# Kernel tuning notes

Hardware: AMD Instinct MI355X
Metric: run time of the kernel (lower is better)

## Reference

```python
import jax, jax.numpy as jnp
import numpy as np

NUM_HEADS = 12


def setup_inputs() -> dict:
    key = jax.random.key(0)
    ks = jax.random.split(key, 5)
    B, N, C = 4, 2048, 768
    s = 0.02
    return {
        "x": jax.random.normal(ks[0], (B, N, C), jnp.float32),
        "qkv_w": jax.random.normal(ks[1], (3 * C, C), jnp.float32) * s,
        "qkv_b": jax.random.normal(ks[2], (3 * C,), jnp.float32) * s,
        "proj_w": jax.random.normal(ks[3], (C, C), jnp.float32) * s,
        "proj_b": jax.random.normal(ks[4], (C,), jnp.float32) * s,
    }


def reference(x, qkv_w, qkv_b, proj_w, proj_b):
    B, N, C = x.shape
    H = NUM_HEADS
    D = C // H
    scale = D ** -0.5
    # qkv projection: [B,N,3C] -> [3,B,H,N,D]
    qkv = (x @ qkv_w.T + qkv_b).reshape(B, N, 3, H, D).transpose(2, 0, 3, 1, 4)
    q, k, v = qkv[0], qkv[1], qkv[2]
    attn = jnp.einsum("bhnd,bhmd->bhnm", q, k) * scale  # [B,H,N,N]
    attn_probs = jax.nn.softmax(attn, axis=-1)
    # dropout p=0 (eval) -> identity
    out = jnp.einsum("bhnm,bhmd->bhnd", attn_probs, v)  # [B,H,N,D]
    out = out.transpose(0, 2, 1, 3).reshape(B, N, C)
    return out @ proj_w.T + proj_b
```

## Files before the change

### kernel.cpp

```cpp
#include <hip/hip_runtime.h>

typedef __attribute__((ext_vector_type(8))) short bf16x8;
typedef __attribute__((ext_vector_type(4))) float f32x4;
typedef __attribute__((ext_vector_type(4))) unsigned int u32x4;
typedef __attribute__((ext_vector_type(2))) unsigned int u32x2;

#define QSCALE 0.1803368801111243f

__device__ inline unsigned short f2bf(float f) {
  union { float f; unsigned u; } v; v.f = f;
  unsigned r = v.u + 0x7fffu + ((v.u >> 16) & 1u);
  return (unsigned short)(r >> 16);
}

__device__ inline unsigned packbf2(float a, float b) {
  union { float f; unsigned u; } va, vb; va.f = a; vb.f = b;
  unsigned ta = va.u + 0x7fffu + ((va.u >> 16) & 1u);
  unsigned tb = vb.u + 0x7fffu + ((vb.u >> 16) & 1u);
  return __builtin_amdgcn_perm(tb, ta, 0x07060302);
}

__device__ inline void async16(const void* g, void* l) {
  __builtin_amdgcn_global_load_lds(
      (const __attribute__((address_space(1))) unsigned int*)g,
      (__attribute__((address_space(3))) unsigned int*)l, 16, 0, 0);
}

__device__ inline void cast8(const float* __restrict__ s, unsigned short* __restrict__ d) {
  float4 v0 = *(const float4*)s, v1 = *(const float4*)(s + 4);
  u32x4 o;
  o.x = packbf2(v0.x, v0.y); o.y = packbf2(v0.z, v0.w);
  o.z = packbf2(v1.x, v1.y); o.w = packbf2(v1.z, v1.w);
  *(u32x4*)d = o;
}

__global__ __launch_bounds__(256) void cast_x(const float* __restrict__ x,
                                              unsigned short* __restrict__ xs) {
  size_t idx = (size_t)blockIdx.x * 256 + threadIdx.x;
  cast8(x + idx * 8, xs + idx * 8);
}

__global__ __launch_bounds__(256) void cast_w(const float* __restrict__ wq,
                                              const float* __restrict__ wp,
                                              unsigned short* __restrict__ wqs,
                                              unsigned short* __restrict__ wps) {
  int idx = blockIdx.x * 256 + threadIdx.x;
  if (idx < 221184) cast8(wq + (size_t)idx * 8, wqs + (size_t)idx * 8);
  else {
    size_t j = (size_t)(idx - 221184) * 8;
    cast8(wp + j, wps + j);
  }
}

template<int MODE>
__global__ __launch_bounds__(256, 3) void gemm_lds(
    const unsigned short* __restrict__ A, const unsigned short* __restrict__ B,
    const float* __restrict__ bias,
    unsigned short* __restrict__ oq, unsigned short* __restrict__ ok,
    unsigned short* __restrict__ ov, float* __restrict__ of)
{
  constexpr int NI = (MODE == 0) ? 4 : 2;
  constexpr int TN = NI * 32;
  __shared__ unsigned short As[128 * 64];
  __shared__ unsigned short Bs[TN * 64];

  const int t = threadIdx.x, w = t >> 6, lane = t & 63;
  const int quad = lane >> 4, l16 = lane & 15;
  const int bm = blockIdx.x, bn = blockIdx.y;
  const int wr = w >> 1, wc = w & 1;

  const int r_off = lane >> 3;
  const int kb_lin = (lane & 7) << 4;

  const unsigned short* Ag = A + (size_t)(bm * 128) * 768;
  const unsigned short* Bg = B + (size_t)(bn * TN) * 768;

  const unsigned short* ApA[4]; unsigned short* LpA[4];
#pragma unroll
  for (int i = 0; i < 4; i++) {
    int r = w * 32 + i * 8 + r_off;
    int ks = (kb_lin ^ ((r & 7) << 4)) >> 1;
    ApA[i] = Ag + (size_t)r * 768 + ks;
    LpA[i] = As + (w * 32 + i * 8) * 64 + lane * 8;
  }
  const unsigned short* ApB[NI]; unsigned short* LpB[NI];
#pragma unroll
  for (int i = 0; i < NI; i++) {
    int r = w * (TN / 4) + i * 8 + r_off;
    int ks = (kb_lin ^ ((r & 7) << 4)) >> 1;
    ApB[i] = Bg + (size_t)r * 768 + ks;
    LpB[i] = Bs + (w * (TN / 4) + i * 8) * 64 + lane * 8;
  }

  f32x4 acc[4][NI] = {};
  const int swz = (l16 & 7) << 3;

  for (int kt = 0; kt < 12; kt++) {
    __syncthreads();
    const int k0 = kt * 64;
#pragma unroll
    for (int i = 0; i < 4; i++)  async16(ApA[i] + k0, LpA[i]);
#pragma unroll
    for (int i = 0; i < NI; i++) async16(ApB[i] + k0, LpB[i]);
    __syncthreads();

#pragma unroll
    for (int kc = 0; kc < 2; kc++) {
      const int ko = (kc * 32 + quad * 8) ^ swz;
      bf16x8 a[4], b[NI];
#pragma unroll
      for (int mi = 0; mi < 4; mi++)
        a[mi] = *(const bf16x8*)&As[(wr * 64 + mi * 16 + l16) * 64 + ko];
#pragma unroll
      for (int ni = 0; ni < NI; ni++)
        b[ni] = *(const bf16x8*)&Bs[(wc * (TN / 2) + ni * 16 + l16) * 64 + ko];
#pragma unroll
      for (int mi = 0; mi < 4; mi++)
#pragma unroll
        for (int ni = 0; ni < NI; ni++)
          acc[mi][ni] = __builtin_amdgcn_mfma_f32_16x16x32_bf16(a[mi], b[ni],
                                                                acc[mi][ni], 0, 0, 0);
    }
  }

  const int m_base = bm * 128 + wr * 64;
  if (MODE == 0) {
    const int three = (bn * TN) / 768;
    int hh[NI], dd[NI]; float bb[NI];
#pragma unroll
    for (int ni = 0; ni < NI; ni++) {
      int n_g = bn * TN + wc * (TN / 2) + ni * 16 + l16;
      bb[ni] = bias[n_g];
      int rem = n_g - three * 768;
      hh[ni] = rem >> 6; dd[ni] = rem & 63;
    }
    if (three == 2) {
#pragma unroll
      for (int ni = 0; ni < NI; ni++)
#pragma unroll
        for (int mi = 0; mi < 4; mi++) {
          int m0 = m_base + mi * 16 + (quad << 2);
          int b_ = m0 >> 11, ntok = m0 & 2047;
          u32x2 pv;
          pv.x = packbf2(acc[mi][ni][0] + bb[ni], acc[mi][ni][1] + bb[ni]);
          pv.y = packbf2(acc[mi][ni][2] + bb[ni], acc[mi][ni][3] + bb[ni]);
          *(u32x2*)(ov + (((size_t)b_ * 12 + hh[ni]) * 64 + dd[ni]) * 2048 + ntok) = pv;
        }
    } else {
      unsigned short* o = (three == 0) ? oq : ok;
      const float sc = (three == 0) ? QSCALE : 1.f;
#pragma unroll
      for (int mi = 0; mi < 4; mi++)
#pragma unroll
        for (int r = 0; r < 4; r++) {
          int m_g = m_base + mi * 16 + (quad << 2) + r;
          int b_ = m_g >> 11, ntok = m_g & 2047;
          size_t rowb = ((size_t)b_ * 12) * 2048;
#pragma unroll
          for (int ni = 0; ni < NI; ni++) {
            float v = (acc[mi][ni][r] + bb[ni]) * sc;
            o[((rowb + (size_t)hh[ni] * 2048 + ntok) << 6) + dd[ni]] = f2bf(v);
          }
        }
    }
  } else {
#pragma unroll
    for (int ni = 0; ni < NI; ni++) {
      int n_g = bn * TN + wc * (TN / 2) + ni * 16 + l16;
      float bs = bias[n_g];
#pragma unroll
      for (int mi = 0; mi < 4; mi++)
#pragma unroll
        for (int r = 0; r < 4; r++) {
          int m_g = m_base + mi * 16 + (quad << 2) + r;
          of[(size_t)m_g * 768 + n_g] = acc[mi][ni][r] + bs;
        }
    }
  }
}

__global__ __launch_bounds__(256, 3) void flash_attn(
    const unsigned short* __restrict__ Qb, const unsigned short* __restrict__ Kb,
    const unsigned short* __restrict__ Vtb, unsigned short* __restrict__ ao)
{
  __shared__ unsigned short Ks[2][4096];
  __shared__ unsigned short Vs[2][4096];
  const int t = threadIdx.x, w = t >> 6, lane = t & 63;
  const int quad = lane >> 4, l16 = lane & 15;
  const int bh = blockIdx.x, qt = blockIdx.y;
  const unsigned short* Qg = Qb + (size_t)bh * 2048 * 64;
  const unsigned short* Kg = Kb + (size_t)bh * 2048 * 64;
  const unsigned short* Vg = Vtb + (size_t)bh * 2048 * 64;

  bf16x8 bq[2][2];
#pragma unroll
  for (int u = 0; u < 2; u++) {
    int qrow = qt * 128 + w * 32 + u * 16 + l16;
#pragma unroll
    for (int h = 0; h < 2; h++)
      bq[u][h] = *(const bf16x8*)(Qg + (size_t)qrow * 64 + h * 32 + quad * 8);
  }

  const int s0 = t, s1 = 256 + t;
  auto gperm = [](int s) { return (s & 0x23) | ((s & 0x0c) << 1) | ((s & 0x10) >> 2); };
  const size_t koff0 = (size_t)gperm(s0 & 63) * 64 + (s0 >> 6) * 8;
  const size_t koff1 = (size_t)gperm(s1 & 63) * 64 + (s1 >> 6) * 8;
  const size_t voff0 = (size_t)(s0 & 63) * 2048 + (s0 >> 6) * 8;
  const size_t voff1 = (size_t)(s1 & 63) * 2048 + (s1 >> 6) * 8;

  float l_run[2] = {0.f, 0.f};
  f32x4 o_acc[2][4];
#pragma unroll
  for (int u = 0; u < 2; u++)
#pragma unroll
    for (int dt = 0; dt < 4; dt++) o_acc[u][dt] = (f32x4){0.f, 0.f, 0.f, 0.f};

  async16(Kg + koff0, &Ks[0][s0 * 8]);
  async16(Kg + koff1, &Ks[0][s1 * 8]);
  async16(Vg + voff0, &Vs[0][s0 * 8]);
  async16(Vg + voff1, &Vs[0][s1 * 8]);

  for (int kt = 0; kt < 32; kt++) {
    const int p = kt & 1;
    __syncthreads();
    if (kt < 31) {
      const unsigned short* Kn = Kg + (size_t)(kt + 1) * 4096;
      const unsigned short* Vn = Vg + (size_t)(kt + 1) * 64;
      async16(Kn + koff0, &Ks[p ^ 1][s0 * 8]);
      async16(Kn + koff1, &Ks[p ^ 1][s1 * 8]);
      async16(Vn + voff0, &Vs[p ^ 1][s0 * 8]);
      async16(Vn + voff1, &Vs[p ^ 1][s1 * 8]);
    }
    const unsigned short* Kp = &Ks[p][0];
    const unsigned short* Vp = &Vs[p][0];

    f32x4 sv[2][4];
#pragma unroll
    for (int nt = 0; nt < 4; nt++) {
      bf16x8 k0 = *(const bf16x8*)&Kp[((quad) * 64 + nt * 16 + l16) * 8];
      bf16x8 k1 = *(const bf16x8*)&Kp[((4 + quad) * 64 + nt * 16 + l16) * 8];
#pragma unroll
      for (int u = 0; u < 2; u++) {
        f32x4 s_ = {0.f, 0.f, 0.f, 0.f};
        s_ = __builtin_amdgcn_mfma_f32_16x16x32_bf16(k0, bq[u][0], s_, 0, 0, 0);
        s_ = __builtin_amdgcn_mfma_f32_16x16x32_bf16(k1, bq[u][1], s_, 0, 0, 0);
        sv[u][nt] = s_;
      }
    }

    union { unsigned u32[8]; bf16x8 v[2]; } pk[2];
#pragma unroll
    for (int u = 0; u < 2; u++) {
#pragma unroll
      for (int nt = 0; nt < 4; nt++) {
        float p0 = __builtin_amdgcn_exp2f(sv[u][nt][0]);
        float p1 = __builtin_amdgcn_exp2f(sv[u][nt][1]);
        float p2 = __builtin_amdgcn_exp2f(sv[u][nt][2]);
        float p3 = __builtin_amdgcn_exp2f(sv[u][nt][3]);
        l_run[u] += (p0 + p1) + (p2 + p3);
        pk[u].u32[nt * 2]     = packbf2(p0, p1);
        pk[u].u32[nt * 2 + 1] = packbf2(p2, p3);
      }
    }

#pragma unroll
    for (int cc = 0; cc < 2; cc++) {
#pragma unroll
      for (int dt = 0; dt < 4; dt++) {
        bf16x8 a = *(const bf16x8*)&Vp[((cc * 4 + quad) * 64 + dt * 16 + l16) * 8];
#pragma unroll
        for (int u = 0; u < 2; u++)
          o_acc[u][dt] = __builtin_amdgcn_mfma_f32_16x16x32_bf16(a, pk[u].v[cc], o_acc[u][dt], 0, 0, 0);
      }
    }
  }

  float linv[2];
#pragma unroll
  for (int u = 0; u < 2; u++) {
    float l = l_run[u];
    l += __shfl_xor(l, 16, 64);
    l += __shfl_xor(l, 32, 64);
    linv[u] = 1.f / l;
  }

  const int b_ = bh / 12, h = bh - b_ * 12;
#pragma unroll
  for (int u = 0; u < 2; u++) {
    int row = b_ * 2048 + qt * 128 + w * 32 + u * 16 + l16;
    unsigned short* base = ao + (size_t)row * 768 + h * 64 + (quad << 2);
#pragma unroll
    for (int dt = 0; dt < 4; dt++) {
      u32x2 pv;
      pv.x = packbf2(o_acc[u][dt][0] * linv[u], o_acc[u][dt][1] * linv[u]);
      pv.y = packbf2(o_acc[u][dt][2] * linv[u], o_acc[u][dt][3] * linv[u]);
      *(u32x2*)(base + dt * 16) = pv;
    }
  }
}

extern "C" void kernel_launch(void* const* d_in, const int* in_sizes, int n_in,
                              void* d_out, int out_size, void* d_ws, size_t ws_size,
                              hipStream_t stream) {
  const float* x      = (const float*)d_in[0];
  const float* qkv_w  = (const float*)d_in[1];
  const float* qkv_b  = (const float*)d_in[2];
  const float* proj_w = (const float*)d_in[3];
  const float* proj_b = (const float*)d_in[4];
  float* out = (float*)d_out;

  unsigned short* ws  = (unsigned short*)d_ws;
  unsigned short* wqs = ws;
  unsigned short* wps = wqs + 1769472;
  unsigned short* xs  = wps + 589824;
  unsigned short* qb  = xs + 6291456;
  unsigned short* kb  = qb + 6291456;
  unsigned short* vtb = kb + 6291456;
  unsigned short* ao  = vtb + 6291456;

  cast_w<<<1152, 256, 0, stream>>>(qkv_w, proj_w, wqs, wps);
  cast_x<<<3072, 256, 0, stream>>>(x, xs);
  gemm_lds<0><<<dim3(64, 18), 256, 0, stream>>>(xs, wqs, qkv_b, qb, kb, vtb, nullptr);
  flash_attn<<<dim3(48, 16), 256, 0, stream>>>(qb, kb, vtb, ao);
  gemm_lds<1><<<dim3(64, 12), 256, 0, stream>>>(ao, wps, proj_b, nullptr, nullptr, nullptr, out);
}
```

Before: 212.2 us.

## Swap MFMA operands for Q/K epilogue, add setprio and hardware bf16 packing

For Q and K tiles of the QKV GEMM, the MFMA operands are swapped so each lane holds four consecutive head-dim values, which allows vectorized 8-byte bf16 stores and float4 bias loads in place of scalar 2-byte scattered stores. The flash attention kernel wraps its MFMA sections in s_setprio to favour matrix issue across waves. It also replaces the software bf16 rounding with the v_cvt_pk_bf16_f32 instruction and accumulates the row sum as a vector, reducing ALU work in the softmax loop. Risks include extra code size from the branch on swapped operands and small rounding differences from the hardware conversion.

```diff
diff --git a/kernel.cpp b/kernel.cpp
--- a/kernel.cpp
+++ b/kernel.cpp
@@ -18,6 +18,12 @@
   unsigned ta = va.u + 0x7fffu + ((va.u >> 16) & 1u);
   unsigned tb = vb.u + 0x7fffu + ((vb.u >> 16) & 1u);
   return __builtin_amdgcn_perm(tb, ta, 0x07060302);
+}
+
+__device__ inline unsigned cvtpk_bf16(float a, float b) {
+  unsigned r;
+  asm("v_cvt_pk_bf16_f32 %0, %1, %2" : "=v"(r) : "v"(a), "v"(b));
+  return r;
 }
 
 __device__ inline void async16(const void* g, void* l) {
@@ -69,6 +75,8 @@
   const int bm = blockIdx.x, bn = blockIdx.y;
   const int wr = w >> 1, wc = w & 1;
 
+  const bool swapped = (MODE == 0) && (bn < 12);
+
   const int r_off = lane >> 3;
   const int kb_lin = (lane & 7) << 4;
 
@@ -114,54 +122,63 @@
 #pragma unroll
       for (int ni = 0; ni < NI; ni++)
         b[ni] = *(const bf16x8*)&Bs[(wc * (TN / 2) + ni * 16 + l16) * 64 + ko];
-#pragma unroll
-      for (int mi = 0; mi < 4; mi++)
-#pragma unroll
-        for (int ni = 0; ni < NI; ni++)
-          acc[mi][ni] = __builtin_amdgcn_mfma_f32_16x16x32_bf16(a[mi], b[ni],
-                                                                acc[mi][ni], 0, 0, 0);
+      if (swapped) {
+#pragma unroll
+        for (int mi = 0; mi < 4; mi++)
+#pragma unroll
+          for (int ni = 0; ni < NI; ni++)
+            acc[mi][ni] = __builtin_amdgcn_mfma_f32_16x16x32_bf16(b[ni], a[mi],
+                                                                  acc[mi][ni], 0, 0, 0);
+      } else {
+#pragma unroll
+        for (int mi = 0; mi < 4; mi++)
+#pragma unroll
+          for (int ni = 0; ni < NI; ni++)
+            acc[mi][ni] = __builtin_amdgcn_mfma_f32_16x16x32_bf16(a[mi], b[ni],
+                                                                  acc[mi][ni], 0, 0, 0);
+      }
     }
   }
 
   const int m_base = bm * 128 + wr * 64;
   if (MODE == 0) {
-    const int three = (bn * TN) / 768;
-    int hh[NI], dd[NI]; float bb[NI];
-#pragma unroll
-    for (int ni = 0; ni < NI; ni++) {
-      int n_g = bn * TN + wc * (TN / 2) + ni * 16 + l16;
-      bb[ni] = bias[n_g];
-      int rem = n_g - three * 768;
-      hh[ni] = rem >> 6; dd[ni] = rem & 63;
-    }
-    if (three == 2) {
-#pragma unroll
-      for (int ni = 0; ni < NI; ni++)
+    const int three = (bn * 128) / 768;
+    if (three < 2) {
+      unsigned short* o = (three == 0) ? oq : ok;
+      const float sc = (three == 0) ? QSCALE : 1.f;
+#pragma unroll
+      for (int ni = 0; ni < NI; ni++) {
+        int nb = bn * 128 + wc * 64 + ni * 16 + (quad << 2);
+        float4 b4 = *(const float4*)&bias[nb];
+        int rem = nb - three * 768;
+        int h = rem >> 6, d0 = rem & 63;
+#pragma unroll
+        for (int mi = 0; mi < 4; mi++) {
+          int m_g = m_base + mi * 16 + l16;
+          int b_ = m_g >> 11, ntok = m_g & 2047;
+          u32x2 pv;
+          pv.x = packbf2((acc[mi][ni][0] + b4.x) * sc, (acc[mi][ni][1] + b4.y) * sc);
+          pv.y = packbf2((acc[mi][ni][2] + b4.z) * sc, (acc[mi][ni][3] + b4.w) * sc);
+          *(u32x2*)(o + (((size_t)b_ * 12 + h) * 2048 + ntok) * 64 + d0) = pv;
+        }
+      }
+    } else {
+#pragma unroll
+      for (int ni = 0; ni < NI; ni++) {
+        int n_g = bn * 128 + wc * 64 + ni * 16 + l16;
+        float bs = bias[n_g];
+        int rem = n_g - 1536;
+        int h = rem >> 6, d = rem & 63;
 #pragma unroll
         for (int mi = 0; mi < 4; mi++) {
           int m0 = m_base + mi * 16 + (quad << 2);
           int b_ = m0 >> 11, ntok = m0 & 2047;
           u32x2 pv;
-          pv.x = packbf2(acc[mi][ni][0] + bb[ni], acc[mi][ni][1] + bb[ni]);
-          pv.y = packbf2(acc[mi][ni][2] + bb[ni], acc[mi][ni][3] + bb[ni]);
-          *(u32x2*)(ov + (((size_t)b_ * 12 + hh[ni]) * 64 + dd[ni]) * 2048 + ntok) = pv;
+          pv.x = packbf2(acc[mi][ni][0] + bs, acc[mi][ni][1] + bs);
+          pv.y = packbf2(acc[mi][ni][2] + bs, acc[mi][ni][3] + bs);
+          *(u32x2*)(ov + (((size_t)b_ * 12 + h) * 64 + d) * 2048 + ntok) = pv;
         }
-    } else {
-      unsigned short* o = (three == 0) ? oq : ok;
-      const float sc = (three == 0) ? QSCALE : 1.f;
-#pragma unroll
-      for (int mi = 0; mi < 4; mi++)
-#pragma unroll
-        for (int r = 0; r < 4; r++) {
-          int m_g = m_base + mi * 16 + (quad << 2) + r;
-          int b_ = m_g >> 11, ntok = m_g & 2047;
-          size_t rowb = ((size_t)b_ * 12) * 2048;
-#pragma unroll
-          for (int ni = 0; ni < NI; ni++) {
-            float v = (acc[mi][ni][r] + bb[ni]) * sc;
-            o[((rowb + (size_t)hh[ni] * 2048 + ntok) << 6) + dd[ni]] = f2bf(v);
-          }
-        }
+      }
     }
   } else {
 #pragma unroll
@@ -208,12 +225,13 @@
   const size_t voff0 = (size_t)(s0 & 63) * 2048 + (s0 >> 6) * 8;
   const size_t voff1 = (size_t)(s1 & 63) * 2048 + (s1 >> 6) * 8;
 
-  float l_run[2] = {0.f, 0.f};
+  const f32x4 z4 = {0.f, 0.f, 0.f, 0.f};
+  f32x4 lacc[2] = {z4, z4};
   f32x4 o_acc[2][4];
 #pragma unroll
   for (int u = 0; u < 2; u++)
 #pragma unroll
-    for (int dt = 0; dt < 4; dt++) o_acc[u][dt] = (f32x4){0.f, 0.f, 0.f, 0.f};
+    for (int dt = 0; dt < 4; dt++) o_acc[u][dt] = z4;
 
   async16(Kg + koff0, &Ks[0][s0 * 8]);
   async16(Kg + koff1, &Ks[0][s1 * 8]);
@@ -235,18 +253,19 @@
     const unsigned short* Vp = &Vs[p][0];
 
     f32x4 sv[2][4];
+    __builtin_amdgcn_s_setprio(1);
 #pragma unroll
     for (int nt = 0; nt < 4; nt++) {
       bf16x8 k0 = *(const bf16x8*)&Kp[((quad) * 64 + nt * 16 + l16) * 8];
       bf16x8 k1 = *(const bf16x8*)&Kp[((4 + quad) * 64 + nt * 16 + l16) * 8];
 #pragma unroll
       for (int u = 0; u < 2; u++) {
-        f32x4 s_ = {0.f, 0.f, 0.f, 0.f};
-        s_ = __builtin_amdgcn_mfma_f32_16x16x32_bf16(k0, bq[u][0], s_, 0, 0, 0);
+        f32x4 s_ = __builtin_amdgcn_mfma_f32_16x16x32_bf16(k0, bq[u][0], z4, 0, 0, 0);
         s_ = __builtin_amdgcn_mfma_f32_16x16x32_bf16(k1, bq[u][1], s_, 0, 0, 0);
         sv[u][nt] = s_;
       }
     }
+    __builtin_amdgcn_s_setprio(0);
 
     union { unsigned u32[8]; bf16x8 v[2]; } pk[2];
 #pragma unroll
@@ -257,12 +276,13 @@
         float p1 = __builtin_amdgcn_exp2f(sv[u][nt][1]);
         float p2 = __builtin_amdgcn_exp2f(sv[u][nt][2]);
         float p3 = __builtin_amdgcn_exp2f(sv[u][nt][3]);
-        l_run[u] += (p0 + p1) + (p2 + p3);
-        pk[u].u32[nt * 2]     = packbf2(p0, p1);
-        pk[u].u32[nt * 2 + 1] = packbf2(p2, p3);
-      }
-    }
-
+        lacc[u] += (f32x4){p0, p1, p2, p3};
+        pk[u].u32[nt * 2]     = cvtpk_bf16(p0, p1);
+        pk[u].u32[nt * 2 + 1] = cvtpk_bf16(p2, p3);
+      }
+    }
+
+    __builtin_amdgcn_s_setprio(1);
 #pragma unroll
     for (int cc = 0; cc < 2; cc++) {
 #pragma unroll
@@ -273,12 +293,13 @@
           o_acc[u][dt] = __builtin_amdgcn_mfma_f32_16x16x32_bf16(a, pk[u].v[cc], o_acc[u][dt], 0, 0, 0);
       }
     }
+    __builtin_amdgcn_s_setprio(0);
   }
 
   float linv[2];
 #pragma unroll
   for (int u = 0; u < 2; u++) {
-    float l = l_run[u];
+    float l = (lacc[u][0] + lacc[u][1]) + (lacc[u][2] + lacc[u][3]);
     l += __shfl_xor(l, 16, 64);
     l += __shfl_xor(l, 32, 64);
     linv[u] = 1.f / l;
@@ -292,8 +313,8 @@
 #pragma unroll
     for (int dt = 0; dt < 4; dt++) {
       u32x2 pv;
-      pv.x = packbf2(o_acc[u][dt][0] * linv[u], o_acc[u][dt][1] * linv[u]);
-      pv.y = packbf2(o_acc[u][dt][2] * linv[u], o_acc[u][dt][3] * linv[u]);
+      pv.x = cvtpk_bf16(o_acc[u][dt][0] * linv[u], o_acc[u][dt][1] * linv[u]);
+      pv.y = cvtpk_bf16(o_acc[u][dt][2] * linv[u], o_acc[u][dt][3] * linv[u]);
       *(u32x2*)(base + dt * 16) = pv;
     }
   }
```

Measured after the change: 252.3 us. 18.9% more time.
